# Optimization experiments

Measured on AMD Instinct MI355X. Metric: run time of the kernel, lower is better.

The kernel has to match this reference:

```python
import jax, jax.numpy as jnp
import numpy as np


def setup_inputs() -> dict:
    key = jax.random.key(0)
    k1, k2, k3, k4 = jax.random.split(key, 4)
    N, F_IN, F_OUT, C = 8192, 128, 128, 4
    X = jax.random.normal(k1, (N, F_IN), dtype=jnp.float32)
    adjs = jax.random.uniform(k2, (C, N, N), dtype=jnp.float32)
    # xavier_normal std = sqrt(2/(fan_in+fan_out))
    std = (2.0 / (F_IN + F_OUT)) ** 0.5
    W = jax.random.normal(k3, (F_IN, F_OUT), dtype=jnp.float32) * std
    adj_W = jax.random.normal(k4, (C, F_IN, F_OUT), dtype=jnp.float32) * std
    b = jnp.zeros((F_OUT,), dtype=jnp.float32)
    return {"X": X, "adjs": adjs, "W": W, "adj_W": adj_W, "b": b}


def reference(X, adjs, W, adj_W, b):
    # x_part: [N, out]
    x_part = X @ W
    # per-channel message passing: (A_c @ X) @ Wa_c, then relu, then sum over channels
    AX = jnp.einsum('cnm,mf->cnf', adjs, X)          # [C, N, in]
    adj_parts = jax.nn.relu(jnp.einsum('cnf,cfo->cno', AX, adj_W))  # [C, N, out]
    adj_part = adj_parts.sum(axis=0)                  # [N, out]
    total = x_part + adj_part + b
    return jax.nn.relu(total)
```

## Files before the change

### kernel.cpp

```cpp
#include <hip/hip_runtime.h>
#include <cstdint>
#include <cstddef>

#define NN 8192
#define FI 128
#define FO 128
#define NCH 4
#define HK 256
#define NH (NN / HK)

typedef __attribute__((ext_vector_type(8))) __bf16 bf16x8;
typedef __attribute__((ext_vector_type(8))) short short8;
typedef __attribute__((ext_vector_type(4))) float f32x4;

static __device__ __forceinline__ f32x4 mfma16(bf16x8 a, bf16x8 b, f32x4 c) {
  return __builtin_amdgcn_mfma_f32_16x16x32_bf16(a, b, c, 0, 0, 0);
}

static __device__ __forceinline__ unsigned short f2bfu(float f) {
  union { __bf16 h; unsigned short u; } cv;
  cv.h = (__bf16)f;
  return cv.u;
}

static __device__ __forceinline__ unsigned int pack2(float a, float b) {
  return (unsigned int)f2bfu(a) | ((unsigned int)f2bfu(b) << 16);
}

__global__ void gcs_pack_x(const float* __restrict__ X, unsigned short* __restrict__ PX) {
  int gid = blockIdx.x * 256 + threadIdx.x;
  int l   = gid & 63;
  int g   = gid >> 6;
  int kk  = g & 255;
  int nt  = g >> 8;
  int col = nt * 16 + (l & 15);
  int k0  = kk * 32 + (l >> 4) * 8;
  unsigned int w[4];
#pragma unroll
  for (int p = 0; p < 4; ++p)
    w[p] = pack2(X[(size_t)(k0 + 2 * p) * FI + col], X[(size_t)(k0 + 2 * p + 1) * FI + col]);
  ((uint4*)PX)[g * 64 + l] = make_uint4(w[0], w[1], w[2], w[3]);
}

__global__ void gcs_pack_w(const float* __restrict__ AW, unsigned short* __restrict__ PW) {
  int gid = blockIdx.x * 256 + threadIdx.x;
  int l   = gid & 63;
  int g   = gid >> 6;
  int ks  = g & 3;
  int ot  = (g >> 2) & 7;
  int c   = g >> 5;
  const float* base = AW + (size_t)c * FI * FO;
  int col = ot * 16 + (l & 15);
  int k0  = ks * 32 + (l >> 4) * 8;
  unsigned int w[4];
#pragma unroll
  for (int p = 0; p < 4; ++p)
    w[p] = pack2(base[(k0 + 2 * p) * FO + col], base[(k0 + 2 * p + 1) * FO + col]);
  ((uint4*)PW)[g * 64 + l] = make_uint4(w[0], w[1], w[2], w[3]);
}

__global__ void gcs_xpart(const float* __restrict__ X, const float* __restrict__ W,
                          const float* __restrict__ b, float* __restrict__ xp) {
  int gid = blockIdx.x * 256 + threadIdx.x;
  int n = gid >> 7;
  int o = gid & 127;
  const float4* Xr = (const float4*)(X + (size_t)n * FI);
  float s = b[o];
#pragma unroll 4
  for (int f4 = 0; f4 < FI / 4; ++f4) {
    float4 xv = Xr[f4];
    s += xv.x * W[(f4 * 4 + 0) * FO + o];
    s += xv.y * W[(f4 * 4 + 1) * FO + o];
    s += xv.z * W[(f4 * 4 + 2) * FO + o];
    s += xv.w * W[(f4 * 4 + 3) * FO + o];
  }
  xp[gid] = s;
}

__global__ void __launch_bounds__(512, 2)
gcs_main(const float* __restrict__ adjs, const unsigned short* __restrict__ PX,
         const unsigned short* __restrict__ PW, const float* __restrict__ xpart,
         float* __restrict__ out) {
  const int rt  = blockIdx.x;
  const int tid = threadIdx.x;
  const int w   = tid >> 6;
  const int l   = tid & 63;
  const int lr  = l & 15;
  const int lk  = l >> 4;

  __shared__ unsigned short buf[2][NCH * 32 * HK];

  f32x4 acc[NCH][2] = {};
  f32x4 pf[16];

#define LOADH(h2)                                                              \
  _Pragma("unroll") for (int j = 0; j < 16; ++j) {                             \
    int p = w * 16 + j; int c = p >> 5; int r = p & 31;                        \
    const float* src = adjs + (size_t)c * NN * NN +                            \
                       (size_t)(rt * 32 + r) * NN + (size_t)(h2) * HK + l * 4; \
    pf[j] = __builtin_nontemporal_load((const f32x4*)src);                     \
  }

#define CVTSTORE(dst)                                                          \
  _Pragma("unroll") for (int j = 0; j < 16; ++j) {                             \
    int p = w * 16 + j; int c = p >> 5; int r = p & 31;                        \
    unsigned int w0 = pack2(pf[j][0], pf[j][1]);                               \
    unsigned int w1 = pack2(pf[j][2], pf[j][3]);                               \
    int byte = c * 16384 + ((r * 512 + l * 8) ^ ((r & 7) << 4));               \
    *(uint2*)((char*)(dst) + byte) = make_uint2(w0, w1);                       \
  }

  LOADH(0);
  CVTSTORE(buf[0]);
  LOADH(1);
  __syncthreads();

  for (int h = 0; h < NH; ++h) {
    const char* bufC = (const char*)buf[h & 1];
#pragma unroll
    for (int s = 0; s < 8; ++s) {
      int kkG = h * 8 + s;
      bf16x8 B = *(const bf16x8*)((const char*)PX + ((size_t)(w * 256 + kkG) * 64 + l) * 16);
#pragma unroll
      for (int c = 0; c < NCH; ++c) {
#pragma unroll
        for (int m = 0; m < 2; ++m) {
          int r = m * 16 + lr;
          int byte = c * 16384 + ((r * 512 + s * 64 + lk * 16) ^ ((r & 7) << 4));
          bf16x8 A = __builtin_bit_cast(bf16x8, *(const short8*)(bufC + byte));
          acc[c][m] = mfma16(A, B, acc[c][m]);
        }
      }
    }
    if (h + 1 < NH) {
      CVTSTORE(buf[(h + 1) & 1]);
      if (h + 2 < NH) { LOADH(h + 2); }
    }
    __syncthreads();
  }

  char* AXs = (char*)buf;
  f32x4 osum0 = {}, osum1 = {};
#pragma unroll
  for (int c = 0; c < NCH; ++c) {
    __syncthreads();
#pragma unroll
    for (int m = 0; m < 2; ++m) {
#pragma unroll
      for (int rr = 0; rr < 4; ++rr) {
        int row = m * 16 + lk * 4 + rr;
        int col = w * 16 + lr;
        int byte = (row * 256 + col * 2) ^ ((row & 7) << 4);
        *(unsigned short*)(AXs + byte) = f2bfu(acc[c][m][rr]);
      }
    }
    __syncthreads();
    f32x4 p0 = {}, p1 = {};
#pragma unroll
    for (int ks = 0; ks < 4; ++ks) {
      int kb = ks * 64 + lk * 16;
      int r0 = lr, r1 = 16 + lr;
      int b0 = (r0 * 256 + kb) ^ ((r0 & 7) << 4);
      int b1 = (r1 * 256 + kb) ^ ((r1 & 7) << 4);
      bf16x8 a0 = __builtin_bit_cast(bf16x8, *(const short8*)(AXs + b0));
      bf16x8 a1 = __builtin_bit_cast(bf16x8, *(const short8*)(AXs + b1));
      bf16x8 bw = *(const bf16x8*)((const char*)PW + ((size_t)(c * 32 + w * 4 + ks) * 64 + l) * 16);
      p0 = mfma16(a0, bw, p0);
      p1 = mfma16(a1, bw, p1);
    }
#pragma unroll
    for (int rr = 0; rr < 4; ++rr) {
      osum0[rr] += fmaxf(p0[rr], 0.0f);
      osum1[rr] += fmaxf(p1[rr], 0.0f);
    }
  }

#pragma unroll
  for (int m = 0; m < 2; ++m) {
#pragma unroll
    for (int rr = 0; rr < 4; ++rr) {
      int row = rt * 32 + m * 16 + lk * 4 + rr;
      int col = w * 16 + lr;
      float s = (m == 0 ? osum0[rr] : osum1[rr]) + xpart[(size_t)row * FO + col];
      out[(size_t)row * FO + col] = fmaxf(s, 0.0f);
    }
  }
}

extern "C" void kernel_launch(void* const* d_in, const int* in_sizes, int n_in,
                              void* d_out, int out_size, void* d_ws, size_t ws_size,
                              hipStream_t stream) {
  const float* X    = (const float*)d_in[0];
  const float* adjs = (const float*)d_in[1];
  const float* W    = (const float*)d_in[2];
  const float* AW   = (const float*)d_in[3];
  const float* b    = (const float*)d_in[4];
  float* out = (float*)d_out;

  char* ws = (char*)d_ws;
  float*          xpart = (float*)ws;
  unsigned short* PX    = (unsigned short*)(ws + (4u << 20));
  unsigned short* PW    = (unsigned short*)(ws + (6u << 20));

  hipLaunchKernelGGL(gcs_pack_x, dim3(512),  dim3(256), 0, stream, X, PX);
  hipLaunchKernelGGL(gcs_pack_w, dim3(32),   dim3(256), 0, stream, AW, PW);
  hipLaunchKernelGGL(gcs_xpart,  dim3(4096), dim3(256), 0, stream, X, W, b, xpart);
  hipLaunchKernelGGL(gcs_main,   dim3(256),  dim3(512), 0, stream, adjs, PX, PW, xpart, out);
}
```

Baseline: 209.6 us.

## Fuse prep kernels, compute x-part via MFMA in main, restructure adjacency streaming

Merges the X and weight packing kernels into one prep launch and also packs W into bf16. The separate fp32 x-part kernel is removed, and X@W plus bias is computed with MFMA in the epilogue of the main kernel. The main loop now streams adjacency two channels at a time over 512-column chunks, alternating between two channel-pair buffers. This cuts launch count and the xpart round trip through global memory. The cost is bf16 precision on X@W and a different load pattern, where each row read now spans 2KB.

```diff
diff --git a/kernel.cpp b/kernel.cpp
--- a/kernel.cpp
+++ b/kernel.cpp
@@ -6,8 +6,6 @@
 #define FI 128
 #define FO 128
 #define NCH 4
-#define HK 256
-#define NH (NN / HK)
 
 typedef __attribute__((ext_vector_type(8))) __bf16 bf16x8;
 typedef __attribute__((ext_vector_type(8))) short short8;
@@ -27,60 +25,51 @@
   return (unsigned int)f2bfu(a) | ((unsigned int)f2bfu(b) << 16);
 }
 
-__global__ void gcs_pack_x(const float* __restrict__ X, unsigned short* __restrict__ PX) {
-  int gid = blockIdx.x * 256 + threadIdx.x;
-  int l   = gid & 63;
-  int g   = gid >> 6;
-  int kk  = g & 255;
-  int nt  = g >> 8;
-  int col = nt * 16 + (l & 15);
-  int k0  = kk * 32 + (l >> 4) * 8;
-  unsigned int w[4];
-#pragma unroll
-  for (int p = 0; p < 4; ++p)
-    w[p] = pack2(X[(size_t)(k0 + 2 * p) * FI + col], X[(size_t)(k0 + 2 * p + 1) * FI + col]);
-  ((uint4*)PX)[g * 64 + l] = make_uint4(w[0], w[1], w[2], w[3]);
-}
-
-__global__ void gcs_pack_w(const float* __restrict__ AW, unsigned short* __restrict__ PW) {
-  int gid = blockIdx.x * 256 + threadIdx.x;
-  int l   = gid & 63;
-  int g   = gid >> 6;
-  int ks  = g & 3;
-  int ot  = (g >> 2) & 7;
-  int c   = g >> 5;
-  const float* base = AW + (size_t)c * FI * FO;
-  int col = ot * 16 + (l & 15);
-  int k0  = ks * 32 + (l >> 4) * 8;
-  unsigned int w[4];
-#pragma unroll
-  for (int p = 0; p < 4; ++p)
-    w[p] = pack2(base[(k0 + 2 * p) * FO + col], base[(k0 + 2 * p + 1) * FO + col]);
-  ((uint4*)PW)[g * 64 + l] = make_uint4(w[0], w[1], w[2], w[3]);
-}
-
-__global__ void gcs_xpart(const float* __restrict__ X, const float* __restrict__ W,
-                          const float* __restrict__ b, float* __restrict__ xp) {
-  int gid = blockIdx.x * 256 + threadIdx.x;
-  int n = gid >> 7;
-  int o = gid & 127;
-  const float4* Xr = (const float4*)(X + (size_t)n * FI);
-  float s = b[o];
-#pragma unroll 4
-  for (int f4 = 0; f4 < FI / 4; ++f4) {
-    float4 xv = Xr[f4];
-    s += xv.x * W[(f4 * 4 + 0) * FO + o];
-    s += xv.y * W[(f4 * 4 + 1) * FO + o];
-    s += xv.z * W[(f4 * 4 + 2) * FO + o];
-    s += xv.w * W[(f4 * 4 + 3) * FO + o];
-  }
-  xp[gid] = s;
+static __device__ __forceinline__ bf16x8 cvt8v(f32x4 a, f32x4 b) {
+  bf16x8 v;
+  v[0] = (__bf16)a[0]; v[1] = (__bf16)a[1]; v[2] = (__bf16)a[2]; v[3] = (__bf16)a[3];
+  v[4] = (__bf16)b[0]; v[5] = (__bf16)b[1]; v[6] = (__bf16)b[2]; v[7] = (__bf16)b[3];
+  return v;
+}
+
+__global__ void gcs_prep(const float* __restrict__ X, const float* __restrict__ AW,
+                         const float* __restrict__ W,
+                         unsigned short* __restrict__ PX, unsigned short* __restrict__ PW) {
+  if (blockIdx.x < 512) {
+    int gid = blockIdx.x * 256 + threadIdx.x;
+    int l   = gid & 63;
+    int g   = gid >> 6;
+    int kk  = g & 255;
+    int nt  = g >> 8;
+    int col = nt * 16 + (l & 15);
+    int k0  = kk * 32 + (l >> 4) * 8;
+    unsigned int w[4];
+#pragma unroll
+    for (int p = 0; p < 4; ++p)
+      w[p] = pack2(X[(size_t)(k0 + 2 * p) * FI + col], X[(size_t)(k0 + 2 * p + 1) * FI + col]);
+    ((uint4*)PX)[g * 64 + l] = make_uint4(w[0], w[1], w[2], w[3]);
+  } else {
+    int gid = (blockIdx.x - 512) * 256 + threadIdx.x;
+    int l   = gid & 63;
+    int g   = gid >> 6;
+    int ks  = g & 3;
+    int ot  = (g >> 2) & 7;
+    int c   = g >> 5;
+    const float* base = (c < 4) ? (AW + (size_t)c * FI * FO) : W;
+    int col = ot * 16 + (l & 15);
+    int k0  = ks * 32 + (l >> 4) * 8;
+    unsigned int w[4];
+#pragma unroll
+    for (int p = 0; p < 4; ++p)
+      w[p] = pack2(base[(k0 + 2 * p) * FO + col], base[(k0 + 2 * p + 1) * FO + col]);
+    ((uint4*)PW)[g * 64 + l] = make_uint4(w[0], w[1], w[2], w[3]);
+  }
 }
 
 __global__ void __launch_bounds__(512, 2)
 gcs_main(const float* __restrict__ adjs, const unsigned short* __restrict__ PX,
-         const unsigned short* __restrict__ PW, const float* __restrict__ xpart,
-         float* __restrict__ out) {
+         const unsigned short* __restrict__ PW, const float* __restrict__ X,
+         const float* __restrict__ b, float* __restrict__ out) {
   const int rt  = blockIdx.x;
   const int tid = threadIdx.x;
   const int w   = tid >> 6;
@@ -88,53 +77,62 @@
   const int lr  = l & 15;
   const int lk  = l >> 4;
 
-  __shared__ unsigned short buf[2][NCH * 32 * HK];
+  __shared__ unsigned short buf[2][2 * 32 * 512];
 
   f32x4 acc[NCH][2] = {};
   f32x4 pf[16];
 
-#define LOADH(h2)                                                              \
-  _Pragma("unroll") for (int j = 0; j < 16; ++j) {                             \
-    int p = w * 16 + j; int c = p >> 5; int r = p & 31;                        \
-    const float* src = adjs + (size_t)c * NN * NN +                            \
-                       (size_t)(rt * 32 + r) * NN + (size_t)(h2) * HK + l * 4; \
-    pf[j] = __builtin_nontemporal_load((const f32x4*)src);                     \
+#define LOADH(par, kq)                                                         \
+  _Pragma("unroll") for (int j = 0; j < 8; ++j) {                              \
+    int p = w * 8 + j; int cc = p >> 5; int r = p & 31;                        \
+    const float* src = adjs + (size_t)((par) * 2 + cc) * NN * NN +             \
+        (size_t)(rt * 32 + r) * NN + (size_t)(kq) * 512 + l * 4;               \
+    pf[j * 2 + 0] = __builtin_nontemporal_load((const f32x4*)src);             \
+    pf[j * 2 + 1] = __builtin_nontemporal_load((const f32x4*)(src + 256));     \
   }
 
 #define CVTSTORE(dst)                                                          \
-  _Pragma("unroll") for (int j = 0; j < 16; ++j) {                             \
-    int p = w * 16 + j; int c = p >> 5; int r = p & 31;                        \
-    unsigned int w0 = pack2(pf[j][0], pf[j][1]);                               \
-    unsigned int w1 = pack2(pf[j][2], pf[j][3]);                               \
-    int byte = c * 16384 + ((r * 512 + l * 8) ^ ((r & 7) << 4));               \
-    *(uint2*)((char*)(dst) + byte) = make_uint2(w0, w1);                       \
-  }
-
-  LOADH(0);
+  _Pragma("unroll") for (int j = 0; j < 8; ++j) {                              \
+    int p = w * 8 + j; int cc = p >> 5; int r = p & 31;                        \
+    _Pragma("unroll") for (int q = 0; q < 2; ++q) {                            \
+      unsigned int w0 = pack2(pf[j * 2 + q][0], pf[j * 2 + q][1]);             \
+      unsigned int w1 = pack2(pf[j * 2 + q][2], pf[j * 2 + q][3]);             \
+      int byte = cc * 32768 + ((r * 1024 + q * 512 + l * 8) ^ ((r & 7) << 4)); \
+      *(uint2*)((char*)(dst) + byte) = make_uint2(w0, w1);                     \
+    }                                                                          \
+  }
+
+#define COMPUTE(bufp, kq, c0, c1)                                              \
+  _Pragma("unroll") for (int s = 0; s < 16; ++s) {                             \
+    bf16x8 B = *(const bf16x8*)((const char*)PX +                              \
+        ((size_t)(w * 256 + (kq) * 16 + s) * 64 + l) * 16);                    \
+    _Pragma("unroll") for (int m = 0; m < 2; ++m) {                            \
+      int r = m * 16 + lr;                                                     \
+      int byt = (r * 1024 + s * 64 + lk * 16) ^ ((r & 7) << 4);                \
+      bf16x8 A0 = __builtin_bit_cast(bf16x8,                                   \
+          *(const short8*)((const char*)(bufp) + byt));                        \
+      bf16x8 A1 = __builtin_bit_cast(bf16x8,                                   \
+          *(const short8*)((const char*)(bufp) + 32768 + byt));                \
+      acc[c0][m] = mfma16(A0, B, acc[c0][m]);                                  \
+      acc[c1][m] = mfma16(A1, B, acc[c1][m]);                                  \
+    }                                                                          \
+  }
+
+  LOADH(0, 0);
   CVTSTORE(buf[0]);
-  LOADH(1);
+  LOADH(1, 0);
   __syncthreads();
 
-  for (int h = 0; h < NH; ++h) {
-    const char* bufC = (const char*)buf[h & 1];
-#pragma unroll
-    for (int s = 0; s < 8; ++s) {
-      int kkG = h * 8 + s;
-      bf16x8 B = *(const bf16x8*)((const char*)PX + ((size_t)(w * 256 + kkG) * 64 + l) * 16);
-#pragma unroll
-      for (int c = 0; c < NCH; ++c) {
-#pragma unroll
-        for (int m = 0; m < 2; ++m) {
-          int r = m * 16 + lr;
-          int byte = c * 16384 + ((r * 512 + s * 64 + lk * 16) ^ ((r & 7) << 4));
-          bf16x8 A = __builtin_bit_cast(bf16x8, *(const short8*)(bufC + byte));
-          acc[c][m] = mfma16(A, B, acc[c][m]);
-        }
-      }
-    }
-    if (h + 1 < NH) {
-      CVTSTORE(buf[(h + 1) & 1]);
-      if (h + 2 < NH) { LOADH(h + 2); }
+  for (int hh = 0; hh < 16; ++hh) {
+    COMPUTE(buf[0], hh, 0, 1);
+    CVTSTORE(buf[1]);
+    if (hh < 15) LOADH(0, hh + 1);
+    __syncthreads();
+
+    COMPUTE(buf[1], hh, 2, 3);
+    if (hh < 15) {
+      CVTSTORE(buf[0]);
+      LOADH(1, hh + 1);
     }
     __syncthreads();
   }
@@ -164,7 +162,8 @@
       int b1 = (r1 * 256 + kb) ^ ((r1 & 7) << 4);
       bf16x8 a0 = __builtin_bit_cast(bf16x8, *(const short8*)(AXs + b0));
       bf16x8 a1 = __builtin_bit_cast(bf16x8, *(const short8*)(AXs + b1));
-      bf16x8 bw = *(const bf16x8*)((const char*)PW + ((size_t)(c * 32 + w * 4 + ks) * 64 + l) * 16);
+      bf16x8 bw = *(const bf16x8*)((const char*)PW +
+          ((size_t)(c * 32 + w * 4 + ks) * 64 + l) * 16);
       p0 = mfma16(a0, bw, p0);
       p1 = mfma16(a1, bw, p1);
     }
@@ -175,16 +174,38 @@
     }
   }
 
+  f32x4 xp0 = {}, xp1 = {};
+#pragma unroll
+  for (int ks = 0; ks < 4; ++ks) {
+    bf16x8 bw = *(const bf16x8*)((const char*)PW +
+        ((size_t)(128 + w * 4 + ks) * 64 + l) * 16);
+#pragma unroll
+    for (int m = 0; m < 2; ++m) {
+      int row_g = rt * 32 + m * 16 + lr;
+      const float* px = X + (size_t)row_g * FI + ks * 32 + lk * 8;
+      f32x4 xa = *(const f32x4*)px;
+      f32x4 xb = *(const f32x4*)(px + 4);
+      bf16x8 a = cvt8v(xa, xb);
+      if (m == 0) xp0 = mfma16(a, bw, xp0);
+      else        xp1 = mfma16(a, bw, xp1);
+    }
+  }
+
+  float bias = b[w * 16 + lr];
 #pragma unroll
   for (int m = 0; m < 2; ++m) {
 #pragma unroll
     for (int rr = 0; rr < 4; ++rr) {
       int row = rt * 32 + m * 16 + lk * 4 + rr;
       int col = w * 16 + lr;
-      float s = (m == 0 ? osum0[rr] : osum1[rr]) + xpart[(size_t)row * FO + col];
+      float s = (m == 0 ? osum0[rr] : osum1[rr]) +
+                (m == 0 ? xp0[rr]   : xp1[rr]) + bias;
       out[(size_t)row * FO + col] = fmaxf(s, 0.0f);
     }
   }
+#undef LOADH
+#undef CVTSTORE
+#undef COMPUTE
 }
 
 extern "C" void kernel_launch(void* const* d_in, const int* in_sizes, int n_in,
@@ -198,12 +219,9 @@
   float* out = (float*)d_out;
 
   char* ws = (char*)d_ws;
-  float*          xpart = (float*)ws;
-  unsigned short* PX    = (unsigned short*)(ws + (4u << 20));
-  unsigned short* PW    = (unsigned short*)(ws + (6u << 20));
-
-  hipLaunchKernelGGL(gcs_pack_x, dim3(512),  dim3(256), 0, stream, X, PX);
-  hipLaunchKernelGGL(gcs_pack_w, dim3(32),   dim3(256), 0, stream, AW, PW);
-  hipLaunchKernelGGL(gcs_xpart,  dim3(4096), dim3(256), 0, stream, X, W, b, xpart);
-  hipLaunchKernelGGL(gcs_main,   dim3(256),  dim3(512), 0, stream, adjs, PX, PW, xpart, out);
-}
+  unsigned short* PX = (unsigned short*)ws;
+  unsigned short* PW = (unsigned short*)(ws + (2u << 20));
+
+  hipLaunchKernelGGL(gcs_prep, dim3(552), dim3(256), 0, stream, X, AW, W, PX, PW);
+  hipLaunchKernelGGL(gcs_main, dim3(256), dim3(512), 0, stream, adjs, PX, PW, X, b, out);
+}
```

Result: slower. 255.0 us (+21.7%).
